# Kernel tuning notes

Measured on AMD Instinct MI355X. Metric: run time of the kernel, lower is better.

## Reference

```python
import jax, jax.numpy as jnp
import numpy as np

N = 20000   # nodes (spots)
E = 100000  # edges (kNN spatial graph, avg degree 5)
IN = 256    # input feature dim = out_dim[-1]
D = 512     # per-head output dim = in_dim (gene count)
H = 4       # heads
NEG_SLOPE = 0.2  # DGL GATv2Conv default negative_slope; fc LeakyReLU slope is also 0.2


def setup_inputs() -> dict:
    key = jax.random.key(0)
    ks = jax.random.split(key, 10)
    s = 0.02
    return {
        "z": jax.random.normal(ks[0], (N, IN), jnp.float32),
        "src": jax.random.randint(ks[1], (E,), 0, N, jnp.int32),
        "dst": jax.random.randint(ks[2], (E,), 0, N, jnp.int32),
        "W_src": jax.random.normal(ks[3], (IN, H * D), jnp.float32) * s,
        "b_src": jnp.zeros((H * D,), jnp.float32),
        "W_dst": jax.random.normal(ks[4], (IN, H * D), jnp.float32) * s,
        "b_dst": jnp.zeros((H * D,), jnp.float32),
        "attn": jax.random.normal(ks[5], (H, D), jnp.float32) * s,
        "gat_bias": jnp.zeros((H * D,), jnp.float32),
        "W_fc": jax.random.normal(ks[6], (H * D, D), jnp.float32) * s,
        "b_fc": jnp.zeros((D,), jnp.float32),
    }


def reference(z, src, dst, W_src, b_src, W_dst, b_dst, attn, gat_bias, W_fc, b_fc):
    # GATv2Conv (DGL semantics, share_weights=False, eval mode so dropout is identity)
    feat_src = (z @ W_src + b_src).reshape(N, H, D)  # [N,H,D]
    feat_dst = (z @ W_dst + b_dst).reshape(N, H, D)  # [N,H,D]
    # per-edge GATv2 score: a^T LeakyReLU(Wsrc h_u + Wdst h_v)
    e = jax.nn.leaky_relu(feat_src[src] + feat_dst[dst], NEG_SLOPE)  # [E,H,D]
    score = jnp.einsum('ehd,hd->eh', e, attn)                        # [E,H]
    # edge softmax over incoming edges of each dst node (numerically stable)
    m = jax.lax.stop_gradient(
        jnp.full((N, H), -jnp.inf, score.dtype).at[dst].max(score))
    ex = jnp.exp(score - m[dst])                                     # [E,H]
    denom = jnp.zeros((N, H), ex.dtype).at[dst].add(ex)              # [N,H]
    alpha = ex / denom[dst]                                          # [E,H]
    # scatter-aggregate messages
    msg = alpha[:, :, None] * feat_src[src]                          # [E,H,D]
    rst = jnp.zeros((N, H, D), msg.dtype).at[dst].add(msg)
    rst = rst + gat_bias.reshape(1, H, D)
    # flatten heads, then fused Linear + LeakyReLU(0.2)
    flat = rst.reshape(N, H * D)
    return jax.nn.leaky_relu(flat @ W_fc + b_fc, NEG_SLOPE)          # [N,D]
```

## Files before the change

### kernel.cpp

```cpp
#include <hip/hip_runtime.h>
#include <hip/hip_bf16.h>
#include <math.h>

#define H_HEADS 4
#define D_HEAD 512
#define HD 2048
#define IN_DIM 256
#define OUTD 512
#define NEG 0.2f

typedef __hip_bfloat16 bf16;
typedef _Float16 f16;
typedef __attribute__((ext_vector_type(2))) _Float16 h2v;
typedef __attribute__((ext_vector_type(8))) short s16x8;
typedef __attribute__((ext_vector_type(4))) float f32x4;

__device__ __forceinline__ float bflo(unsigned w) { union { unsigned u; float f; } x; x.u = w << 16; return x.f; }
__device__ __forceinline__ float bfhi(unsigned w) { union { unsigned u; float f; } x; x.u = w & 0xffff0000u; return x.f; }

template<int MODE>
__device__ __forceinline__ void gemm_body(char* smem_raw,
                      const bf16* __restrict__ A, int lda, long aOff,
                      const bf16* __restrict__ Bt, int ldb, long bOff,
                      const float* __restrict__ bias, long biasOff,
                      const float* __restrict__ bias2, const int* __restrict__ rowptr,
                      void* __restrict__ Cv, int ldc, long cOff,
                      int M, int K, int bx, int by, int z)
{
    bf16* stg = (bf16*)smem_raw;

    const int tid  = threadIdx.x;
    const int r0   = by * 128;
    const int n0   = bx * 128;
    const int lane = tid & 63;
    const int wave = tid >> 6;
    const int wr   = (wave >> 1) * 64;
    const int wc   = (wave & 1) * 64;
    const int l15  = lane & 15;
    const int quad = lane >> 4;

    const bf16* Az = A + aOff * (long)z;
    const bf16* Bz = Bt + bOff * (long)z;

    f32x4 acc[4][4];
    #pragma unroll
    for (int i = 0; i < 4; i++)
        #pragma unroll
        for (int j = 0; j < 4; j++)
            #pragma unroll
            for (int r = 0; r < 4; r++) acc[i][j][r] = 0.f;

    const int srow = tid >> 2;
    const int skof = (((tid & 3) ^ ((srow >> 1) & 3)) * 8);
    const int swz  = (l15 >> 1) & 3;

    auto stage_tile = [&](int c, int k0) {
        bf16* As = stg + c * 8192;
        bf16* Bs = As + 4096;
        #pragma unroll
        for (int p = 0; p < 2; p++) {
            int ar = r0 + p * 64 + srow;
            if (ar >= M) ar = M - 1;
            const bf16* ga = Az + (size_t)ar * lda + k0 + skof;
            __builtin_amdgcn_global_load_lds(
                (const __attribute__((address_space(1))) void*)ga,
                (__attribute__((address_space(3))) void*)(As + (p * 256 + tid) * 8),
                16, 0, 0);
            const bf16* gb = Bz + (size_t)(n0 + p * 64 + srow) * ldb + k0 + skof;
            __builtin_amdgcn_global_load_lds(
                (const __attribute__((address_space(1))) void*)gb,
                (__attribute__((address_space(3))) void*)(Bs + (p * 256 + tid) * 8),
                16, 0, 0);
        }
    };

    stage_tile(0, 0);
    int cbuf = 0;
    for (int k0 = 0; k0 < K; k0 += 32) {
        __syncthreads();
        if (k0 + 32 < K) stage_tile(cbuf ^ 1, k0 + 32);

        const bf16* As = stg + cbuf * 8192;
        const bf16* Bs = As + 4096;
        s16x8 af[4], bg[4];
        #pragma unroll
        for (int i = 0; i < 4; i++)
            af[i] = *(const s16x8*)(As + (wr + i * 16 + l15) * 32 + (quad ^ swz) * 8);
        #pragma unroll
        for (int j = 0; j < 4; j++)
            bg[j] = *(const s16x8*)(Bs + (wc + j * 16 + l15) * 32 + (quad ^ swz) * 8);
        #pragma unroll
        for (int i = 0; i < 4; i++)
            #pragma unroll
            for (int j = 0; j < 4; j++)
                acc[i][j] = __builtin_amdgcn_mfma_f32_16x16x32_bf16(af[i], bg[j], acc[i][j], 0, 0, 0);
        cbuf ^= 1;
    }
    __syncthreads();

    if (MODE == 0 || MODE == 2) {
        float bv[4];
        #pragma unroll
        for (int j = 0; j < 4; j++)
            bv[j] = bias ? bias[biasOff * (long)z + n0 + wc + j * 16 + l15] : 0.f;

        const long cb = cOff * (long)z;

        if (MODE == 0) {
            bf16* Cs = (bf16*)smem_raw;
            #pragma unroll
            for (int i = 0; i < 4; i++)
                #pragma unroll
                for (int j = 0; j < 4; j++)
                    #pragma unroll
                    for (int r = 0; r < 4; r++)
                        Cs[(wr + i * 16 + quad * 4 + r) * 136 + wc + j * 16 + l15] =
                            __float2bfloat16(acc[i][j][r] + bv[j]);
        } else {
            f16* Cs = (f16*)smem_raw;
            #pragma unroll
            for (int i = 0; i < 4; i++)
                #pragma unroll
                for (int j = 0; j < 4; j++)
                    #pragma unroll
                    for (int r = 0; r < 4; r++)
                        Cs[(wr + i * 16 + quad * 4 + r) * 136 + wc + j * 16 + l15] =
                            (f16)(acc[i][j][r] + bv[j]);
        }
        __syncthreads();
        #pragma unroll
        for (int it = 0; it < 8; it++) {
            const int idx  = it * 256 + tid;
            const int lrow = idx >> 4;
            const int lcol = (idx & 15) * 8;
            const int grow = r0 + lrow;
            if (grow < M)
                *(uint4*)((short*)Cv + cb + (size_t)grow * ldc + n0 + lcol) =
                    *(const uint4*)((const short*)smem_raw + lrow * 136 + lcol);
        }
    } else {
        float* C = (float*)Cv;
        float* Csf = (float*)smem_raw;

        #pragma unroll
        for (int p = 0; p < 2; p++) {
            __syncthreads();
            if (wr == p * 64) {
                #pragma unroll
                for (int i = 0; i < 4; i++)
                    #pragma unroll
                    for (int j = 0; j < 4; j++)
                        #pragma unroll
                        for (int r = 0; r < 4; r++)
                            Csf[(i * 16 + quad * 4 + r) * 132 + wc + j * 16 + l15] = acc[i][j][r];
            }
            __syncthreads();
            #pragma unroll
            for (int it = 0; it < 8; it++) {
                const int idx  = it * 256 + tid;
                const int lrow = idx >> 5;
                const int lcol = (idx & 31) * 4;
                const int grow = r0 + p * 64 + lrow;
                if (grow < M) {
                    const int gcol = n0 + lcol;
                    float4 v  = *(const float4*)(Csf + lrow * 132 + lcol);
                    const float4 c4 = *(const float4*)(bias + gcol);
                    const float4 b4 = *(const float4*)(bias2 + gcol);
                    const bool has = rowptr[grow + 1] > rowptr[grow];
                    v.x += c4.x + (has ? b4.x : 0.f);
                    v.y += c4.y + (has ? b4.y : 0.f);
                    v.z += c4.z + (has ? b4.z : 0.f);
                    v.w += c4.w + (has ? b4.w : 0.f);
                    v.x = v.x > 0.f ? v.x : NEG * v.x;
                    v.y = v.y > 0.f ? v.y : NEG * v.y;
                    v.z = v.z > 0.f ? v.z : NEG * v.z;
                    v.w = v.w > 0.f ? v.w : NEG * v.w;
                    *(float4*)(C + (size_t)grow * ldc + gcol) = v;
                }
            }
        }
    }
}

__device__ __forceinline__ int xcd_swizzle_flat()
{
    const int nwg = gridDim.x * gridDim.y * gridDim.z;
    int f = blockIdx.x + gridDim.x * (blockIdx.y + gridDim.y * blockIdx.z);
    const int xcd = f & 7;
    const int i   = f >> 3;
    const int q = nwg >> 3, r = nwg & 7;
    return (xcd < r ? xcd * (q + 1) : r * (q + 1) + (xcd - r) * q) + i;
}

template<int MODE>
__global__ __launch_bounds__(256)
void mfma_gemm_kernel(const bf16* __restrict__ A, int lda, long aOff,
                      const bf16* __restrict__ Bt, int ldb, long bOff,
                      const float* __restrict__ bias, long biasOff,
                      const float* __restrict__ bias2, const int* __restrict__ rowptr,
                      void* __restrict__ Cv, int ldc, long cOff,
                      int M, int K)
{
    constexpr int SMEM_BYTES = (MODE == 1) ? (64 * 132 * 4) : (128 * 136 * 2);
    static_assert(SMEM_BYTES >= 4 * 4096 * 2, "staging dbuf must fit");
    __shared__ __align__(16) char smem_raw[SMEM_BYTES];
    const int f   = xcd_swizzle_flat();
    const int bx  = f % gridDim.x;
    const int byz = f / gridDim.x;
    gemm_body<MODE>(smem_raw, A, lda, aOff, Bt, ldb, bOff, bias, biasOff,
                    bias2, rowptr, Cv, ldc, cOff, M, K,
                    bx, byz % gridDim.y, byz / gridDim.y);
}

__global__ __launch_bounds__(256)
void fused_gemm02_kernel(int gx, int gy, int nMain,
    const bf16* __restrict__ A2, int lda2, long aOff2,
    const bf16* __restrict__ B2, int ldb2, long bOff2,
    const float* __restrict__ bias2v, long biasOff2,
    void* __restrict__ C2, int ldc2, long cOff2, int M2, int K2,
    const bf16* __restrict__ A0, int lda0, long aOff0,
    const bf16* __restrict__ B0, int ldb0, long bOff0,
    void* __restrict__ C0, int ldc0, long cOff0, int M0, int K0)
{
    __shared__ __align__(16) char smem_raw[128 * 136 * 2];
    const int f = xcd_swizzle_flat();
    if (f < 32) {
        const int bx0 = f & 1;
        const int by0 = (f >> 1) & 3;
        const int z0  = f >> 3;
        gemm_body<0>(smem_raw, A0, lda0, aOff0, B0, ldb0, bOff0, nullptr, 0,
                     nullptr, nullptr, C0, ldc0, cOff0, M0, K0, bx0, by0, z0);
    } else {
        const int fm = f - 32;
        const int bx = fm % gx;
        const int t  = fm / gx;
        gemm_body<2>(smem_raw, A2, lda2, aOff2, B2, ldb2, bOff2, bias2v, biasOff2,
                     nullptr, nullptr, C2, ldc2, cOff2, M2, K2, bx, t % gy, t / gy);
    }
}

__global__ __launch_bounds__(256)
void prep_kernel(const float* __restrict__ W_src, const float* __restrict__ W_dst,
                 const float* __restrict__ W_fc, const float* __restrict__ b_src,
                 const float* __restrict__ b_dst, const float* __restrict__ attn,
                 const float* __restrict__ b_fc, const float* __restrict__ gat_bias,
                 bf16* __restrict__ WsbT, bf16* __restrict__ WdbT,
                 bf16* __restrict__ WfcT, bf16* __restrict__ Wsb,
                 float* __restrict__ bias_cat, f16* __restrict__ atn16,
                 int* __restrict__ cnt, int nCnt,
                 float* __restrict__ cvec, float* __restrict__ bsW_tot, int miscB)
{
    __shared__ float tile[32][33];
    const int b   = blockIdx.x;
    const int tid = threadIdx.x;
    const int tx  = tid & 31;
    const int ty0 = tid >> 5;

    if (b < 1024) {
        const float* In = (b < 512) ? W_src : W_dst;
        bf16* Out       = (b < 512) ? WsbT : WdbT;
        const int a  = b & 511;
        const int bk = a & 7;
        const int bn = a >> 3;
        #pragma unroll
        for (int i = 0; i < 4; i++) {
            const int r = ty0 + i * 8;
            tile[r][tx] = In[(size_t)(bk * 32 + r) * HD + bn * 32 + tx];
        }
        __syncthreads();
        #pragma unroll
        for (int i = 0; i < 4; i++) {
            const int r = ty0 + i * 8;
            Out[(size_t)(bn * 32 + r) * IN_DIM + bk * 32 + tx] = __float2bfloat16(tile[tx][r]);
        }
        return;
    }
    if (b < 2048) {
        const int c  = b - 1024;
        const int h  = c >> 8;
        const int r8 = c & 255;
        const int bt = r8 & 15;
        const int bj = r8 >> 4;
        #pragma unroll
        for (int i = 0; i < 4; i++) {
            const int r = ty0 + i * 8;
            tile[r][tx] = W_fc[(size_t)(h * 512 + bt * 32 + r) * OUTD + bj * 32 + tx];
        }
        __syncthreads();
        #pragma unroll
        for (int i = 0; i < 4; i++) {
            const int r = ty0 + i * 8;
            WfcT[(size_t)(h * 512 + bj * 32 + r) * 512 + bt * 32 + tx] = __float2bfloat16(tile[tx][r]);
        }
        return;
    }
    if (b < 2560) {
        const int i4 = ((b - 2048) * 256 + tid) * 4;
        const float4 v = *(const float4*)(W_src + i4);
        Wsb[i4 + 0] = __float2bfloat16(v.x);
        Wsb[i4 + 1] = __float2bfloat16(v.y);
        Wsb[i4 + 2] = __float2bfloat16(v.z);
        Wsb[i4 + 3] = __float2bfloat16(v.w);
        return;
    }
    if (b < 2560 + miscB) {
        int idx = (b - 2560) * 256 + tid;
        if (idx < 2 * HD) { bias_cat[idx] = (idx < HD) ? b_src[idx] : b_dst[idx - HD]; return; }
        idx -= 2 * HD;
        if (idx < HD) { atn16[idx] = (f16)attn[idx]; return; }
        idx -= HD;
        if (idx < nCnt) cnt[idx] = 0;
        return;
    }
    {
        __shared__ float red[256];
        const int rb = b - (2560 + miscB);
        const bool isCvec = rb < OUTD;
        const int j = isCvec ? rb : rb - OUTD;
        const float* vec = isCvec ? gat_bias : b_src;
        float s = 0.f;
        for (int k = tid; k < HD; k += 256)
            s = fmaf(vec[k], W_fc[(size_t)k * OUTD + j], s);
        red[tid] = s;
        __syncthreads();
        for (int o = 128; o > 0; o >>= 1) {
            if (tid < o) red[tid] += red[tid + o];
            __syncthreads();
        }
        if (tid == 0) {
            if (isCvec) cvec[j] = red[0] + b_fc[j];
            else bsW_tot[j] = red[0];
        }
    }
}

__global__ void cast_hist_kernel(const float* __restrict__ S, bf16* __restrict__ T,
                                 long n4, const int* __restrict__ dst,
                                 int* __restrict__ cnt, int E)
{
    long t = (long)blockIdx.x * 256 + threadIdx.x;
    if (t < n4) {
        const long i = t * 4;
        const float4 v = *(const float4*)(S + i);
        T[i + 0] = __float2bfloat16(v.x);
        T[i + 1] = __float2bfloat16(v.y);
        T[i + 2] = __float2bfloat16(v.z);
        T[i + 3] = __float2bfloat16(v.w);
        return;
    }
    t -= n4;
    if (t < E) atomicAdd(&cnt[dst[t]], 1);
}

__global__ __launch_bounds__(256)
void scan_lookback_kernel(const int* __restrict__ cnt, int* __restrict__ rowptr,
                          int* __restrict__ cursor, int* __restrict__ flags, int n)
{
    __shared__ int ws[4];
    __shared__ int exoff_s;
    const int tid  = threadIdx.x;
    const int lane = tid & 63;
    const int wv   = tid >> 6;
    const int b    = blockIdx.x;
    const int i    = b * 256 + tid;
    int v = (i < n) ? cnt[i] : 0;
    #pragma unroll
    for (int d = 1; d < 64; d <<= 1) {
        const int t = __shfl_up(v, d, 64);
        if (lane >= d) v += t;
    }
    if (lane == 63) ws[wv] = v;
    __syncthreads();
    int s = 0;
    if (wv > 0) s += ws[0];
    if (wv > 1) s += ws[1];
    if (wv > 2) s += ws[2];
    const int incl = v + s;
    if (tid == 255)
        atomicExch(&flags[b], incl + 1);
    if (wv == 0) {
        int acc = 0;
        for (int idx = lane; idx < b; idx += 64) {
            int r;
            do { r = atomicAdd(&flags[idx], 0); } while (r == 0);
            acc += r - 1;
        }
        #pragma unroll
        for (int ofs = 32; ofs > 0; ofs >>= 1)
            acc += __shfl_xor(acc, ofs, 64);
        if (lane == 0) exoff_s = acc;
    }
    __syncthreads();
    const int r = incl + exoff_s;
    if (i < n) {
        rowptr[i + 1] = r;
        if (i + 1 < n) cursor[i + 1] = r;
    }
    if (b == 0 && tid == 0) { rowptr[0] = 0; cursor[0] = 0; }
}

__global__ void scatter_kernel(const int* __restrict__ src, const int* __restrict__ dst,
                               int* __restrict__ cursor, int* __restrict__ csr_src, int E)
{
    const int e = blockIdx.x * 256 + threadIdx.x;
    if (e >= E) return;
    const int pos = atomicAdd(&cursor[dst[e]], 1);
    csr_src[pos] = src[e];
}

__device__ __forceinline__ _Float16 score_head_pk(const uint4 pa, const uint4 pb, const uint4 at)
{
    const unsigned* ua = (const unsigned*)&pa;
    const unsigned* ub = (const unsigned*)&pb;
    const unsigned* ut = (const unsigned*)&at;
    h2v acc = (h2v)(_Float16)0.f;
    const h2v c06 = (h2v)(_Float16)0.6f;
    const h2v c04 = (h2v)(_Float16)0.4f;
    #pragma unroll
    for (int c = 0; c < 4; c++) {
        union { unsigned u; h2v h; } A, B, T, S, Ab;
        A.u = ua[c]; B.u = ub[c]; T.u = ut[c];
        S.h = A.h + B.h;
        Ab.u = S.u & 0x7fff7fffu;
        const h2v l = S.h * c06 + Ab.h * c04;
        acc += l * T.h;
    }
    return acc.x + acc.y;
}

__device__ __forceinline__ float score_head_h2(const uint4 pa, const uint4 pb, const uint4 at)
{
    const unsigned* ua = (const unsigned*)&pa;
    const unsigned* ub = (const unsigned*)&pb;
    const unsigned* ut = (const unsigned*)&at;
    h2v acc = (h2v)(_Float16)0.f;
    const h2v c06 = (h2v)(_Float16)0.6f;
    const h2v c04 = (h2v)(_Float16)0.4f;
    #pragma unroll
    for (int c = 0; c < 4; c++) {
        union { unsigned u; h2v h; } A, B, T, S, Ab;
        A.u = ua[c]; B.u = ub[c]; T.u = ut[c];
        S.h = A.h + B.h;
        Ab.u = S.u & 0x7fff7fffu;
        const h2v l = S.h * c06 + Ab.h * c04;
        acc += l * T.h;
    }
    return (float)acc.x + (float)acc.y;
}

__global__ __launch_bounds__(256)
void score_agg_kernel(const f16* __restrict__ fs, const f16* __restrict__ fd,
                      const bf16* __restrict__ zb,
                      const int* __restrict__ rowptr, const int* __restrict__ csr_src,
                      const f16* __restrict__ atn16, bf16* __restrict__ agg, int N)
{
    const int h    = threadIdx.x >> 6;
    const int lane = threadIdx.x & 63;
    const int v    = blockIdx.x;
    if (v >= N) return;

    const uint4 at = *(const uint4*)(atn16 + h * D_HEAD + lane * 8);
    const f16* fsh = fs + h * D_HEAD + (size_t)lane * 8;

    const int off0 = rowptr[v], off1 = rowptr[v + 1];
    const int deg  = off1 - off0;
    float acc[4] = {0.f, 0.f, 0.f, 0.f};
    float den = 0.f;

    const uint4 fdr = *(const uint4*)(fd + (size_t)v * HD + h * D_HEAD + lane * 8);

    for (int e = 0; e < deg; e += 4) {
        const int i0 = off0 + e;
        const int i1 = off0 + ((e + 1 < deg) ? e + 1 : e);
        const int i2 = off0 + ((e + 2 < deg) ? e + 2 : e);
        const int i3 = off0 + ((e + 3 < deg) ? e + 3 : e);
        const int u0 = csr_src[i0], u1 = csr_src[i1], u2 = csr_src[i2], u3 = csr_src[i3];

        const uint4 pa0 = *(const uint4*)(fsh + (size_t)u0 * HD);
        const uint4 pa1 = *(const uint4*)(fsh + (size_t)u1 * HD);
        const uint4 pa2 = *(const uint4*)(fsh + (size_t)u2 * HD);
        const uint4 pa3 = *(const uint4*)(fsh + (size_t)u3 * HD);
        const uint2 z0 = *(const uint2*)(zb + (size_t)u0 * IN_DIM + lane * 4);
        const uint2 z1 = *(const uint2*)(zb + (size_t)u1 * IN_DIM + lane * 4);
        const uint2 z2 = *(const uint2*)(zb + (size_t)u2 * IN_DIM + lane * 4);
        const uint2 z3 = *(const uint2*)(zb + (size_t)u3 * IN_DIM + lane * 4);

        union { unsigned u; h2v h; } w01, w23;
        w01.h.x = score_head_pk(pa0, fdr, at);
        w01.h.y = score_head_pk(pa1, fdr, at);
        w23.h.x = score_head_pk(pa2, fdr, at);
        w23.h.y = score_head_pk(pa3, fdr, at);
        #pragma unroll
        for (int ofs = 32; ofs > 0; ofs >>= 1) {
            union { int i; h2v h; } t01, t23;
            t01.i = __shfl_xor((int)w01.u, ofs, 64);
            t23.i = __shfl_xor((int)w23.u, ofs, 64);
            w01.h += t01.h;
            w23.h += t23.h;
        }
        const float s0 = (float)w01.h.x;
        const float s1 = (float)w01.h.y;
        const float s2 = (float)w23.h.x;
        const float s3 = (float)w23.h.y;
        const float e0 = __expf(s0);
        const float e1 = (e + 1 < deg) ? __expf(s1) : 0.f;
        const float e2 = (e + 2 < deg) ? __expf(s2) : 0.f;
        const float e3 = (e + 3 < deg) ? __expf(s3) : 0.f;
        den += e0 + e1 + e2 + e3;
        const float zc0[4] = {bflo(z0.x), bfhi(z0.x), bflo(z0.y), bfhi(z0.y)};
        const float zc1[4] = {bflo(z1.x), bfhi(z1.x), bflo(z1.y), bfhi(z1.y)};
        const float zc2[4] = {bflo(z2.x), bfhi(z2.x), bflo(z2.y), bfhi(z2.y)};
        const float zc3[4] = {bflo(z3.x), bfhi(z3.x), bflo(z3.y), bfhi(z3.y)};
        #pragma unroll
        for (int c = 0; c < 4; c++)
            acc[c] += (e0 * zc0[c] + e1 * zc1[c]) + (e2 * zc2[c] + e3 * zc3[c]);
    }
    if (deg > 0) {
        const float inv = 1.f / den;
        #pragma unroll
        for (int c = 0; c < 4; c++) acc[c] *= inv;
    }

    union { uint2 u; short s[4]; } pk;
    #pragma unroll
    for (int c = 0; c < 4; c++) {
        const bf16 b = __float2bfloat16(acc[c]);
        pk.s[c] = *(const short*)&b;
    }
    *(uint2*)(agg + (size_t)v * (H_HEADS * IN_DIM) + h * IN_DIM + lane * 4) = pk.u;
}

__global__ __launch_bounds__(256)
void score_csr_kernel(const f16* __restrict__ fs, const f16* __restrict__ fd,
                      const int* __restrict__ rowptr, const int* __restrict__ csr_src,
                      const f16* __restrict__ atn16, float* __restrict__ expbuf,
                      float* __restrict__ denomB, int N)
{
    const int wave = threadIdx.x >> 6;
    const int lane = threadIdx.x & 63;
    const int wgid = blockIdx.x * 4 + wave;
    const int nw   = gridDim.x * 4;

    uint4 at[H_HEADS];
    #pragma unroll
    for (int h = 0; h < H_HEADS; h++)
        at[h] = *(const uint4*)(atn16 + h * D_HEAD + lane * 8);

    for (int v = wgid; v < N; v += nw) {
        const int off0 = rowptr[v], off1 = rowptr[v + 1];
        if (off0 == off1) continue;
        uint4 fdr[H_HEADS];
        #pragma unroll
        for (int h = 0; h < H_HEADS; h++)
            fdr[h] = *(const uint4*)(fd + (size_t)v * HD + h * D_HEAD + lane * 8);

        float4 den = make_float4(0.f, 0.f, 0.f, 0.f);
        for (int o = off0; o < off1; o += 2) {
            const bool two = (o + 1 < off1);
            const int u0 = csr_src[o];
            const int u1 = two ? csr_src[o + 1] : u0;
            const f16* f0 = fs + (size_t)u0 * HD + lane * 8;
            const f16* f1 = fs + (size_t)u1 * HD + lane * 8;
            uint4 pa0[H_HEADS], pa1[H_HEADS];
            #pragma unroll
            for (int h = 0; h < H_HEADS; h++) pa0[h] = *(const uint4*)(f0 + h * D_HEAD);
            #pragma unroll
            for (int h = 0; h < H_HEADS; h++) pa1[h] = *(const uint4*)(f1 + h * D_HEAD);

            float s0[H_HEADS], s1[H_HEADS];
            #pragma unroll
            for (int h = 0; h < H_HEADS; h++) {
                s0[h] = score_head_h2(pa0[h], fdr[h], at[h]);
                s1[h] = score_head_h2(pa1[h], fdr[h], at[h]);
            }
            #pragma unroll
            for (int ofs = 32; ofs > 0; ofs >>= 1) {
                #pragma unroll
                for (int h = 0; h < H_HEADS; h++) {
                    s0[h] += __shfl_xor(s0[h], ofs, 64);
                    s1[h] += __shfl_xor(s1[h], ofs, 64);
                }
            }
            const float4 e0 = make_float4(expf(s0[0]), expf(s0[1]), expf(s0[2]), expf(s0[3]));
            den.x += e0.x; den.y += e0.y; den.z += e0.z; den.w += e0.w;
            float4 e1;
            if (two) {
                e1 = make_float4(expf(s1[0]), expf(s1[1]), expf(s1[2]), expf(s1[3]));
                den.x += e1.x; den.y += e1.y; den.z += e1.z; den.w += e1.w;
            }
            if (lane == 0) {
                *(float4*)(expbuf + (size_t)o * H_HEADS) = e0;
                if (two) *(float4*)(expbuf + (size_t)(o + 1) * H_HEADS) = e1;
            }
        }
        if (lane == 0) *(float4*)(denomB + (size_t)v * H_HEADS) = den;
    }
}

__global__ __launch_bounds__(256)
void agg_z_kernel(const bf16* __restrict__ zb, const int* __restrict__ rowptr,
                  const int* __restrict__ csr_src, const float* __restrict__ expbuf,
                  const float* __restrict__ denomB, bf16* __restrict__ agg, int N)
{
    const int wave = threadIdx.x >> 6;
    const int lane = threadIdx.x & 63;
    const int wgid = blockIdx.x * 4 + wave;
    const int nw   = gridDim.x * 4;

    for (int v = wgid; v < N; v += nw) {
        const int off0 = rowptr[v], off1 = rowptr[v + 1];
        float acc[H_HEADS][4];
        #pragma unroll
        for (int h = 0; h < H_HEADS; h++)
            #pragma unroll
            for (int c = 0; c < 4; c++) acc[h][c] = 0.f;

        if (off1 > off0) {
            const float4 den = *(const float4*)(denomB + (size_t)v * H_HEADS);
            const float4 inv = make_float4(1.f / den.x, 1.f / den.y, 1.f / den.z, 1.f / den.w);
            int o = off0;
            for (; o + 1 < off1; o += 2) {
                const float4 e0 = *(const float4*)(expbuf + (size_t)o * H_HEADS);
                const float4 e1 = *(const float4*)(expbuf + (size_t)(o + 1) * H_HEADS);
                const int u0 = csr_src[o], u1 = csr_src[o + 1];
                const uint2 z0 = *(const uint2*)(zb + (size_t)u0 * IN_DIM + lane * 4);
                const uint2 z1 = *(const uint2*)(zb + (size_t)u1 * IN_DIM + lane * 4);
                const float a0[4] = {e0.x * inv.x, e0.y * inv.y, e0.z * inv.z, e0.w * inv.w};
                const float a1[4] = {e1.x * inv.x, e1.y * inv.y, e1.z * inv.z, e1.w * inv.w};
                const float zc0[4] = {bflo(z0.x), bfhi(z0.x), bflo(z0.y), bfhi(z0.y)};
                const float zc1[4] = {bflo(z1.x), bfhi(z1.x), bflo(z1.y), bfhi(z1.y)};
                #pragma unroll
                for (int h = 0; h < H_HEADS; h++)
                    #pragma unroll
                    for (int c = 0; c < 4; c++)
                        acc[h][c] += a0[h] * zc0[c] + a1[h] * zc1[c];
            }
            if (o < off1) {
                const float4 e0 = *(const float4*)(expbuf + (size_t)o * H_HEADS);
                const int u0 = csr_src[o];
                const uint2 z0 = *(const uint2*)(zb + (size_t)u0 * IN_DIM + lane * 4);
                const float a0[4] = {e0.x * inv.x, e0.y * inv.y, e0.z * inv.z, e0.w * inv.w};
                const float zc0[4] = {bflo(z0.x), bfhi(z0.x), bflo(z0.y), bfhi(z0.y)};
                #pragma unroll
                for (int h = 0; h < H_HEADS; h++)
                    #pragma unroll
                    for (int c = 0; c < 4; c++)
                        acc[h][c] += a0[h] * zc0[c];
            }
        }
        #pragma unroll
        for (int h = 0; h < H_HEADS; h++) {
            union { uint2 u; short s[4]; } pk;
            #pragma unroll
            for (int c = 0; c < 4; c++) {
                const bf16 b = __float2bfloat16(acc[h][c]);
                pk.s[c] = *(const short*)&b;
            }
            *(uint2*)(agg + (size_t)v * (H_HEADS * IN_DIM) + h * IN_DIM + lane * 4) = pk.u;
        }
    }
}

extern "C" void kernel_launch(void* const* d_in, const int* in_sizes, int n_in,
                              void* d_out, int out_size, void* d_ws, size_t ws_size,
                              hipStream_t stream)
{
    const float* z        = (const float*)d_in[0];
    const int*   src      = (const int*)d_in[1];
    const int*   dst      = (const int*)d_in[2];
    const float* W_src    = (const float*)d_in[3];
    const float* b_src    = (const float*)d_in[4];
    const float* W_dst    = (const float*)d_in[5];
    const float* b_dst    = (const float*)d_in[6];
    const float* attn     = (const float*)d_in[7];
    const float* gat_bias = (const float*)d_in[8];
    const float* W_fc     = (const float*)d_in[9];
    const float* b_fc     = (const float*)d_in[10];
    float* out = (float*)d_out;

    const int N = in_sizes[0] / IN_DIM;
    const int E = in_sizes[1];
    const int nBlocksScan = (N + 255) / 256;

    char* p = (char*)d_ws;
    const size_t featB = (size_t)N * HD * 2;
    f16* fs       = (f16*)p;   p += featB;
    f16* fd       = (f16*)p;   p += featB;
    bf16* zb      = (bf16*)p;  p += (size_t)N * IN_DIM * sizeof(bf16);
    bf16* WsbT    = (bf16*)p;  p += (size_t)HD * IN_DIM * sizeof(bf16);
    bf16* WdbT    = (bf16*)p;  p += (size_t)HD * IN_DIM * sizeof(bf16);
    bf16* Wsb     = (bf16*)p;  p += (size_t)IN_DIM * HD * sizeof(bf16);
    bf16* WfcT    = (bf16*)p;  p += (size_t)HD * D_HEAD * sizeof(bf16);
    bf16* Wfinal  = (bf16*)p;  p += (size_t)OUTD * 1024 * sizeof(bf16);
    float* bias_cat = (float*)p; p += (size_t)2 * HD * sizeof(float);
    f16* atn16    = (f16*)p;   p += (size_t)HD * sizeof(f16);
    float* bsW_tot = (float*)p; p += (size_t)OUTD * sizeof(float);
    float* cvec   = (float*)p; p += (size_t)OUTD * sizeof(float);
    float* expbuf = (float*)p; p += (size_t)E * H_HEADS * sizeof(float);
    float* denomB = (float*)p; p += (size_t)N * H_HEADS * sizeof(float);
    int* cnt      = (int*)p;   p += (size_t)N * 4;
    int* flags    = (int*)p;   p += (size_t)128 * 4;
    int* rowptr   = (int*)p;   p += ((size_t)(N + 1) * 4 + 15) & ~15ULL;
    int* cursor   = (int*)p;   p += ((size_t)N * 4 + 15) & ~15ULL;
    int* csr_src  = (int*)p;   p += ((size_t)E * 4 + 15) & ~15ULL;

    bf16* aggSep = (bf16*)p;
    const size_t needFused = (size_t)(p - (char*)d_ws) + (size_t)N * (H_HEADS * IN_DIM) * sizeof(bf16);
    const bool fused = (ws_size >= needFused);
    bf16* agg = fused ? aggSep : (bf16*)fs;

    const int miscElems = 2 * HD + HD + (N + 128);
    const int miscB = (miscElems + 255) / 256;
    prep_kernel<<<2560 + miscB + 2 * OUTD, 256, 0, stream>>>(
        W_src, W_dst, W_fc, b_src, b_dst, attn, b_fc, gat_bias,
        WsbT, WdbT, WfcT, Wsb, bias_cat, atn16, cnt, N + 128, cvec, bsW_tot, miscB);

    const long n4 = (long)N * IN_DIM / 4;
    cast_hist_kernel<<<(int)((n4 + E + 255) / 256), 256, 0, stream>>>(z, zb, n4, dst, cnt, E);

    scan_lookback_kernel<<<nBlocksScan, 256, 0, stream>>>(cnt, rowptr, cursor, flags, N);
    scatter_kernel<<<(E + 255) / 256, 256, 0, stream>>>(src, dst, cursor, csr_src, E);

    const int gx = HD / 128;
    const int gy = (N + 127) / 128;
    const int nMain = gx * gy * 2;
    fused_gemm02_kernel<<<nMain + 32, 256, 0, stream>>>(
        gx, gy, nMain,
        zb, IN_DIM, 0L,
        WsbT, IN_DIM, (long)HD * IN_DIM,
        bias_cat, (long)HD,
        fs, HD, (long)N * HD,
        N, IN_DIM,
        WfcT, D_HEAD, (long)D_HEAD * D_HEAD,
        Wsb, HD, (long)D_HEAD,
        Wfinal, 1024, (long)IN_DIM,
        D_HEAD, D_HEAD);

    if (fused) {
        score_agg_kernel<<<N, 256, 0, stream>>>(fs, fd, zb, rowptr, csr_src, atn16, agg, N);
    } else {
        score_csr_kernel<<<2500, 256, 0, stream>>>(fs, fd, rowptr, csr_src, atn16, expbuf, denomB, N);
        agg_z_kernel<<<2500, 256, 0, stream>>>(zb, rowptr, csr_src, expbuf, denomB, agg, N);
    }

    mfma_gemm_kernel<1><<<dim3(OUTD / 128, (N + 127) / 128, 1), 256, 0, stream>>>(
        agg, H_HEADS * IN_DIM, 0L,
        Wfinal, H_HEADS * IN_DIM, 0L,
        cvec, 0L, bsW_tot, rowptr,
        out, OUTD, 0L,
        N, H_HEADS * IN_DIM);
}
```

Before: 312.6 us.

## Merge histogram, scan and scatter into one grid-synchronized CSR kernel; fold z cast into prep

```diff
diff --git a/kernel.cpp b/kernel.cpp
--- a/kernel.cpp
+++ b/kernel.cpp
@@ -244,11 +244,13 @@
                  const float* __restrict__ W_fc, const float* __restrict__ b_src,
                  const float* __restrict__ b_dst, const float* __restrict__ attn,
                  const float* __restrict__ b_fc, const float* __restrict__ gat_bias,
+                 const float* __restrict__ zsrc, bf16* __restrict__ zb, long nzb,
                  bf16* __restrict__ WsbT, bf16* __restrict__ WdbT,
                  bf16* __restrict__ WfcT, bf16* __restrict__ Wsb,
                  float* __restrict__ bias_cat, f16* __restrict__ atn16,
                  int* __restrict__ cnt, int nCnt,
-                 float* __restrict__ cvec, float* __restrict__ bsW_tot, int miscB)
+                 float* __restrict__ cvec, float* __restrict__ bsW_tot,
+                 int zcastB, int miscB)
 {
     __shared__ float tile[32][33];
     const int b   = blockIdx.x;
@@ -303,8 +305,19 @@
         Wsb[i4 + 3] = __float2bfloat16(v.w);
         return;
     }
-    if (b < 2560 + miscB) {
-        int idx = (b - 2560) * 256 + tid;
+    if (b < 2560 + zcastB) {
+        const long i = ((long)(b - 2560) * 256 + tid) * 4;
+        if (i < nzb) {
+            const float4 v = *(const float4*)(zsrc + i);
+            zb[i + 0] = __float2bfloat16(v.x);
+            zb[i + 1] = __float2bfloat16(v.y);
+            zb[i + 2] = __float2bfloat16(v.z);
+            zb[i + 3] = __float2bfloat16(v.w);
+        }
+        return;
+    }
+    if (b < 2560 + zcastB + miscB) {
+        int idx = (b - 2560 - zcastB) * 256 + tid;
         if (idx < 2 * HD) { bias_cat[idx] = (idx < HD) ? b_src[idx] : b_dst[idx - HD]; return; }
         idx -= 2 * HD;
         if (idx < HD) { atn16[idx] = (f16)attn[idx]; return; }
@@ -314,7 +327,7 @@
     }
     {
         __shared__ float red[256];
-        const int rb = b - (2560 + miscB);
+        const int rb = b - (2560 + zcastB + miscB);
         const bool isCvec = rb < OUTD;
         const int j = isCvec ? rb : rb - OUTD;
         const float* vec = isCvec ? gat_bias : b_src;
@@ -334,78 +347,79 @@
     }
 }
 
-__global__ void cast_hist_kernel(const float* __restrict__ S, bf16* __restrict__ T,
-                                 long n4, const int* __restrict__ dst,
-                                 int* __restrict__ cnt, int E)
-{
-    long t = (long)blockIdx.x * 256 + threadIdx.x;
-    if (t < n4) {
-        const long i = t * 4;
-        const float4 v = *(const float4*)(S + i);
-        T[i + 0] = __float2bfloat16(v.x);
-        T[i + 1] = __float2bfloat16(v.y);
-        T[i + 2] = __float2bfloat16(v.z);
-        T[i + 3] = __float2bfloat16(v.w);
-        return;
-    }
-    t -= n4;
-    if (t < E) atomicAdd(&cnt[dst[t]], 1);
-}
-
 __global__ __launch_bounds__(256)
-void scan_lookback_kernel(const int* __restrict__ cnt, int* __restrict__ rowptr,
-                          int* __restrict__ cursor, int* __restrict__ flags, int n)
-{
-    __shared__ int ws[4];
-    __shared__ int exoff_s;
+void csr_build_kernel(const int* __restrict__ src, const int* __restrict__ dst,
+                      int* __restrict__ cnt, int* __restrict__ rowptr,
+                      int* __restrict__ cursor, int* __restrict__ csr_src,
+                      int* __restrict__ flags, int* __restrict__ syncv,
+                      int N, int E, int nb, int nScan)
+{
     const int tid  = threadIdx.x;
     const int lane = tid & 63;
     const int wv   = tid >> 6;
     const int b    = blockIdx.x;
-    const int i    = b * 256 + tid;
-    int v = (i < n) ? cnt[i] : 0;
-    #pragma unroll
-    for (int d = 1; d < 64; d <<= 1) {
-        const int t = __shfl_up(v, d, 64);
-        if (lane >= d) v += t;
-    }
-    if (lane == 63) ws[wv] = v;
+
+    for (int e = b * 256 + tid; e < E; e += nb * 256)
+        atomicAdd(&cnt[dst[e]], 1);
     __syncthreads();
-    int s = 0;
-    if (wv > 0) s += ws[0];
-    if (wv > 1) s += ws[1];
-    if (wv > 2) s += ws[2];
-    const int incl = v + s;
-    if (tid == 255)
-        atomicExch(&flags[b], incl + 1);
-    if (wv == 0) {
-        int acc = 0;
-        for (int idx = lane; idx < b; idx += 64) {
-            int r;
-            do { r = atomicAdd(&flags[idx], 0); } while (r == 0);
-            acc += r - 1;
-        }
-        #pragma unroll
-        for (int ofs = 32; ofs > 0; ofs >>= 1)
-            acc += __shfl_xor(acc, ofs, 64);
-        if (lane == 0) exoff_s = acc;
+    if (tid == 0) {
+        __threadfence();
+        atomicAdd(&syncv[0], 1);
+        while (atomicAdd(&syncv[0], 0) < nb) { }
     }
     __syncthreads();
-    const int r = incl + exoff_s;
-    if (i < n) {
-        rowptr[i + 1] = r;
-        if (i + 1 < n) cursor[i + 1] = r;
-    }
-    if (b == 0 && tid == 0) { rowptr[0] = 0; cursor[0] = 0; }
-}
-
-__global__ void scatter_kernel(const int* __restrict__ src, const int* __restrict__ dst,
-                               int* __restrict__ cursor, int* __restrict__ csr_src, int E)
-{
-    const int e = blockIdx.x * 256 + threadIdx.x;
-    if (e >= E) return;
-    const int pos = atomicAdd(&cursor[dst[e]], 1);
-    csr_src[pos] = src[e];
+
+    if (b < nScan) {
+        __shared__ int ws[4];
+        __shared__ int exoff_s;
+        const int i = b * 256 + tid;
+        int v = (i < N) ? atomicAdd(&cnt[i], 0) : 0;
+        #pragma unroll
+        for (int d = 1; d < 64; d <<= 1) {
+            const int t = __shfl_up(v, d, 64);
+            if (lane >= d) v += t;
+        }
+        if (lane == 63) ws[wv] = v;
+        __syncthreads();
+        int s = 0;
+        if (wv > 0) s += ws[0];
+        if (wv > 1) s += ws[1];
+        if (wv > 2) s += ws[2];
+        const int incl = v + s;
+        if (tid == 255)
+            atomicExch(&flags[b], incl + 1);
+        if (wv == 0) {
+            int acc = 0;
+            for (int idx = lane; idx < b; idx += 64) {
+                int r;
+                do { r = atomicAdd(&flags[idx], 0); } while (r == 0);
+                acc += r - 1;
+            }
+            #pragma unroll
+            for (int ofs = 32; ofs > 0; ofs >>= 1)
+                acc += __shfl_xor(acc, ofs, 64);
+            if (lane == 0) exoff_s = acc;
+        }
+        __syncthreads();
+        const int r = incl + exoff_s;
+        if (i < N) {
+            rowptr[i + 1] = r;
+            if (i + 1 < N) atomicExch(&cursor[i + 1], r);
+        }
+        if (b == 0 && tid == 0) { rowptr[0] = 0; atomicExch(&cursor[0], 0); }
+    }
+    __syncthreads();
+    if (tid == 0) {
+        __threadfence();
+        atomicAdd(&syncv[1], 1);
+        while (atomicAdd(&syncv[1], 0) < nb) { }
+    }
+    __syncthreads();
+
+    for (int e = b * 256 + tid; e < E; e += nb * 256) {
+        const int pos = atomicAdd(&cursor[dst[e]], 1);
+        csr_src[pos] = src[e];
+    }
 }
 
 __device__ __forceinline__ _Float16 score_head_pk(const uint4 pa, const uint4 pb, const uint4 at)
@@ -680,7 +694,8 @@
 
     const int N = in_sizes[0] / IN_DIM;
     const int E = in_sizes[1];
-    const int nBlocksScan = (N + 255) / 256;
+    const int nScan  = (N + 255) / 256;
+    const int nEdgeB = (E + 255) / 256;
 
     char* p = (char*)d_ws;
     const size_t featB = (size_t)N * HD * 2;
@@ -700,6 +715,8 @@
     float* denomB = (float*)p; p += (size_t)N * H_HEADS * sizeof(float);
     int* cnt      = (int*)p;   p += (size_t)N * 4;
     int* flags    = (int*)p;   p += (size_t)128 * 4;
+    int* syncv    = (int*)p;   p += (size_t)2 * 4;
+    p = (char*)(((size_t)p + 15) & ~15ULL);
     int* rowptr   = (int*)p;   p += ((size_t)(N + 1) * 4 + 15) & ~15ULL;
     int* cursor   = (int*)p;   p += ((size_t)N * 4 + 15) & ~15ULL;
     int* csr_src  = (int*)p;   p += ((size_t)E * 4 + 15) & ~15ULL;
@@ -709,17 +726,18 @@
     const bool fused = (ws_size >= needFused);
     bf16* agg = fused ? aggSep : (bf16*)fs;
 
-    const int miscElems = 2 * HD + HD + (N + 128);
+    const long nzb = (long)N * IN_DIM;
+    const int zcastB = (int)((nzb / 4 + 255) / 256);
+    const int miscElems = 2 * HD + HD + (N + 128 + 2);
     const int miscB = (miscElems + 255) / 256;
-    prep_kernel<<<2560 + miscB + 2 * OUTD, 256, 0, stream>>>(
+    prep_kernel<<<2560 + zcastB + miscB + 2 * OUTD, 256, 0, stream>>>(
         W_src, W_dst, W_fc, b_src, b_dst, attn, b_fc, gat_bias,
-        WsbT, WdbT, WfcT, Wsb, bias_cat, atn16, cnt, N + 128, cvec, bsW_tot, miscB);
-
-    const long n4 = (long)N * IN_DIM / 4;
-    cast_hist_kernel<<<(int)((n4 + E + 255) / 256), 256, 0, stream>>>(z, zb, n4, dst, cnt, E);
-
-    scan_lookback_kernel<<<nBlocksScan, 256, 0, stream>>>(cnt, rowptr, cursor, flags, N);
-    scatter_kernel<<<(E + 255) / 256, 256, 0, stream>>>(src, dst, cursor, csr_src, E);
+        z, zb, nzb,
+        WsbT, WdbT, WfcT, Wsb, bias_cat, atn16, cnt, N + 128 + 2,
+        cvec, bsW_tot, zcastB, miscB);
+
+    csr_build_kernel<<<nEdgeB, 256, 0, stream>>>(
+        src, dst, cnt, rowptr, cursor, csr_src, flags, syncv, N, E, nEdgeB, nScan);
 
     const int gx = HD / 128;
     const int gy = (N + 127) / 128;
```

Result: slower. 364.4 us (+16.6%).
